# Performance work log

Measured on AMD Instinct MI355X. Metric: run time of the kernel, lower is better.

The kernel has to match this reference:

```python
import jax, jax.numpy as jnp
import numpy as np

N_NODES = 100000
N_EDGES = 3200000
N_GRAPHS = 64


def _seg_mean(vals, idx, num_segments):
    s = jax.ops.segment_sum(vals, idx, num_segments=num_segments)
    cnt = jax.ops.segment_sum(jnp.ones((vals.shape[0],), vals.dtype), idx,
                              num_segments=num_segments)
    return s / jnp.maximum(cnt, 1.0)[:, None]


def _gcn_layer(x, edge_index, edge_attr, Wc, bc, Wn):
    # center = lin1(x)
    center = x @ Wc + bc
    row, col = edge_index[0], edge_index[1]  # row = source (j), col = target (i)
    # degree computed over row indices (as in PyG degree(row))
    deg = jax.ops.segment_sum(jnp.ones((row.shape[0],), x.dtype), row,
                              num_segments=x.shape[0])
    deg_inv_sqrt = jnp.where(deg > 0, jax.lax.rsqrt(jnp.maximum(deg, 1.0)), 0.0)
    norm = deg_inv_sqrt[row] * deg_inv_sqrt[col]  # [E]
    # message: lin2(concat(x_j, edge_attr)) * norm
    msg = jnp.concatenate([x[row], edge_attr], axis=1) @ Wn  # [E, out]
    msg = msg * norm[:, None]
    # aggr='mean' at target nodes
    aggr = _seg_mean(msg, col, x.shape[0])
    return center + aggr


def setup_inputs() -> dict:
    key = jax.random.key(0)
    ks = jax.random.split(key, 12)
    x = jax.random.normal(ks[0], (N_NODES, 3), dtype=jnp.float32)
    edge_index = jax.random.randint(ks[1], (2, N_EDGES), 0, N_NODES, dtype=jnp.int64)
    edge_attr = jax.random.normal(ks[2], (N_EDGES, 2), dtype=jnp.float32)
    batch = jnp.sort(jax.random.randint(ks[3], (N_NODES,), 0, N_GRAPHS, dtype=jnp.int64))
    s = 0.2
    params = {
        'Wc1': jax.random.normal(ks[4], (3, 16), jnp.float32) * s,
        'bc1': jnp.zeros((16,), jnp.float32),
        'Wn1': jax.random.normal(ks[5], (5, 16), jnp.float32) * s,   # in+edge = 3+2
        'Wc2': jax.random.normal(ks[6], (16, 16), jnp.float32) * s,
        'bc2': jnp.zeros((16,), jnp.float32),
        'Wn2': jax.random.normal(ks[7], (18, 16), jnp.float32) * s,  # 16+2
        'Wl1': jax.random.normal(ks[8], (16, 16), jnp.float32) * s,
        'bl1': jnp.zeros((16,), jnp.float32),
        'Wl2': jax.random.normal(ks[9], (16, 2), jnp.float32) * s,
        'bl2': jnp.zeros((2,), jnp.float32),
    }
    return dict(x=x, edge_index=edge_index, edge_attr=edge_attr, batch=batch, **params)


def reference(x, edge_index, edge_attr, batch,
              Wc1, bc1, Wn1, Wc2, bc2, Wn2, Wl1, bl1, Wl2, bl2):
    h = _gcn_layer(x, edge_index, edge_attr, Wc1, bc1, Wn1)
    h = jax.nn.relu(h)  # dropout is identity in eval mode
    h = _gcn_layer(h, edge_index, edge_attr, Wc2, bc2, Wn2)
    h = jax.nn.relu(h)
    g = _seg_mean(h, batch, N_GRAPHS)          # global scatter_mean pooling [G,16]
    g = jax.nn.relu(g @ Wl1 + bl1)
    return g @ Wl2 + bl2                        # [G, 2]
```

## Files before the change

### kernel.cpp

```cpp
#include <hip/hip_runtime.h>

constexpr int TPBW = 1024;
constexpr int TPBS = 256;
constexpr int BSH  = 6;
constexpr int BKN  = 64;
constexpr int MAXB = 1600;
constexpr int CAP  = 2432;
constexpr int SBUF = 2432;
constexpr int ITER = 10;
constexpr int SIT  = 7;
constexpr int SEDG = SIT * TPBW;
constexpr int HWL  = 12800;

__device__ __forceinline__ unsigned short f2bf(float f) {
    unsigned u = __float_as_uint(f);
    u += 0x7FFFu + ((u >> 16) & 1u);
    return (unsigned short)(u >> 16);
}
__device__ __forceinline__ float bflo(unsigned u) {
    return __uint_as_float(u << 16);
}
__device__ __forceinline__ float bfhi(unsigned u) {
    return __uint_as_float(u & 0xFFFF0000u);
}

__global__ __launch_bounds__(TPBW)
void k_stage2(const int* __restrict__ ei, const float2* __restrict__ ea,
              int E, int NBKT, int W,
              int* __restrict__ gcnt, int2* __restrict__ staged,
              unsigned int* __restrict__ partialR) {
    __shared__ unsigned int lh[HWL];
    __shared__ int2 sb2[SEDG];
    __shared__ unsigned short sbk[SEDG];
    __shared__ int cl[MAXB], gb[MAXB], rs[MAXB + 1];
    __shared__ int tmp[1024];
    __shared__ int carry_s;
    const int p = blockIdx.x, t = threadIdx.x;
    for (int i = t; i < W; i += TPBW) lh[i] = 0;
    for (int b = t; b < NBKT; b += TPBW) cl[b] = 0;
    if (t == 0) carry_s = 0;
    __syncthreads();
    const int* colA = ei + E;
    const int s = p * SEDG, send = min(s + SEDG, E);
    int rid[SIT], eap[SIT], bk[SIT], rk[SIT];
#pragma unroll
    for (int k = 0; k < SIT; k++) {
        int e = s + t + k * TPBW;
        bk[k] = -1;
        if (e < send) {
            int r = ei[e], c = colA[e];
            atomicAdd(&lh[r >> 3], 1u << ((r & 7) * 4));
            int b = c >> BSH;
            float2 ev = ea[e];
            rid[k] = (r << BSH) | (c & (BKN - 1));
            eap[k] = (int)((unsigned)f2bf(ev.x) | ((unsigned)f2bf(ev.y) << 16));
            bk[k] = b;
            rk[k] = atomicAdd(&cl[b], 1);
        }
    }
    __syncthreads();
    for (int chunk = 0; chunk < NBKT; chunk += 1024) {
        int idx = chunk + t;
        int v = (idx < NBKT) ? cl[idx] : 0;
        tmp[t] = v;
        __syncthreads();
        for (int off = 1; off < 1024; off <<= 1) {
            int add = (t >= off) ? tmp[t - off] : 0;
            __syncthreads();
            tmp[t] += add;
            __syncthreads();
        }
        int incl = tmp[t];
        int carry = carry_s;
        if (idx < NBKT) rs[idx] = carry + incl - v;
        __syncthreads();
        if (t == 1023) carry_s = carry + incl;
        __syncthreads();
    }
    if (t == 0) rs[NBKT] = carry_s;
    __syncthreads();
    for (int b = t; b < NBKT; b += TPBW) {
        int c = cl[b];
        gb[b] = c ? atomicAdd(&gcnt[b], c) : 0;
    }
    __syncthreads();
#pragma unroll
    for (int k = 0; k < SIT; k++)
        if (bk[k] >= 0) {
            int slot = rs[bk[k]] + rk[k];
            sb2[slot] = make_int2(rid[k], eap[k]);
            sbk[slot] = (unsigned short)bk[k];
        }
    __syncthreads();
    const int total = rs[NBKT];
    for (int i = t; i < total; i += TPBW) {
        int b = sbk[i];
        int pos = gb[b] + (i - rs[b]);
        if (pos < CAP) staged[(size_t)b * CAP + pos] = sb2[i];
    }
    for (int w = t; w < W; w += TPBW) partialR[(size_t)p * W + w] = lh[w];
}

__global__ __launch_bounds__(512)
void k_xd(const unsigned int* __restrict__ partialR, int NP, int W, int N,
          const float* __restrict__ x,
          float* __restrict__ dis, float4* __restrict__ xd) {
    __shared__ unsigned int sA[8][64], sB[8][64];
    const int wloc = threadIdx.x & 63, lane = threadIdx.x >> 6;
    const int w = blockIdx.x * 64 + wloc;
    unsigned int accA = 0, accB = 0;
    if (w < W) {
        for (int p = lane; p < NP; p += 8) {
            unsigned int v = partialR[(size_t)p * W + w];
            accA += v & 0x0F0F0F0Fu;
            accB += (v >> 4) & 0x0F0F0F0Fu;
        }
    }
    sA[lane][wloc] = accA;
    sB[lane][wloc] = accB;
    __syncthreads();
    if (lane == 0 && w < W) {
#pragma unroll
        for (int l = 1; l < 8; l++) { accA += sA[l][wloc]; accB += sB[l][wloc]; }
        int d[8];
        d[0] = accA & 255; d[2] = (accA >> 8) & 255;
        d[4] = (accA >> 16) & 255; d[6] = accA >> 24;
        d[1] = accB & 255; d[3] = (accB >> 8) & 255;
        d[5] = (accB >> 16) & 255; d[7] = accB >> 24;
        const int n0 = w * 8;
#pragma unroll
        for (int k = 0; k < 8; k++) {
            int n = n0 + k;
            if (n < N) {
                float dv = d[k] ? rsqrtf((float)d[k]) : 0.f;
                dis[n] = dv;
                xd[n] = make_float4(x[3 * (size_t)n], x[3 * (size_t)n + 1],
                                    x[3 * (size_t)n + 2], dv);
            }
        }
    }
}

__global__ __launch_bounds__(TPBS)
void k_sortA(int2* __restrict__ staged, const int* __restrict__ gcnt,
             const float4* __restrict__ xd, int N,
             const float* __restrict__ Wc, const float* __restrict__ bc,
             const float* __restrict__ Wn,
             unsigned short* __restrict__ hb, unsigned short* __restrict__ hbs,
             float2* __restrict__ eaS,
             int* __restrict__ cnt, int* __restrict__ base, int* __restrict__ segN) {
    __shared__ int2 sbuf2[SBUF];
    __shared__ int lfill[BKN], lexc[BKN];
    __shared__ float sax[BKN], say[BKN], saz[BKN], se1[BKN], se2[BKN];
    __shared__ float sWc[48], sbc[16], sWn[80];
    __shared__ int stot;
    const int b = blockIdx.x, t = threadIdx.x;
    const size_t s0 = (size_t)b * CAP;
    const int c0 = b << BSH;
    int cb = gcnt[b]; if (cb > CAP) cb = CAP;
    if (t < BKN) lfill[t] = 0;
    if (t < 48) sWc[t] = Wc[t];
    if (t >= 64 && t < 80) sbc[t - 64] = bc[t - 64];
    if (t >= 128 && t < 208) sWn[t - 128] = Wn[t - 128];
    __syncthreads();
    int er[ITER], ep[ITER], rk[ITER];
#pragma unroll
    for (int k = 0; k < ITER; k++) {
        int e = t + k * TPBS;
        rk[k] = -1;
        if (e < cb) {
            int2 v = staged[s0 + e];
            int j = v.x & (BKN - 1);
            er[k] = (int)(((unsigned)v.x) >> BSH);
            ep[k] = v.y;
            rk[k] = atomicAdd(&lfill[j], 1) | (j << 16);
        }
    }
    __syncthreads();
    if (t < 64) {
        int v = lfill[t];
        int incl = v;
#pragma unroll
        for (int off = 1; off < 64; off <<= 1) {
            int up = __shfl_up(incl, off, 64);
            if (t >= off) incl += up;
        }
        lexc[t] = incl - v;
        if (t == 63) stot = incl;
    }
    __syncthreads();
#pragma unroll
    for (int k = 0; k < ITER; k++) {
        if (rk[k] >= 0) {
            int j = rk[k] >> 16, rr = rk[k] & 0xFFFF;
            sbuf2[lexc[j] + rr] = make_int2(er[k], ep[k]);
        }
    }
    __syncthreads();
    int tot = stot; if (tot > SBUF) tot = SBUF;
    const int grp = t >> 2, sub = t & 3;
    const int node = c0 + grp;
    float a0 = 0.f, a1 = 0.f, a2 = 0.f, b1 = 0.f, b2 = 0.f;
    {
        int e0 = lexc[grp], dg = lfill[grp];
        if (node < N) {
            for (int e = sub; e < dg; e += 8) {
                int2 ve0 = sbuf2[e0 + e];
                bool v1 = (e + 4) < dg;
                int2 ve1 = v1 ? sbuf2[e0 + e + 4] : ve0;
                float4 q0 = xd[ve0.x];
                float4 q1 = xd[ve1.x];
                float w0 = q0.w;
                float w1 = v1 ? q1.w : 0.f;
                a0 += w0 * q0.x + w1 * q1.x;
                a1 += w0 * q0.y + w1 * q1.y;
                a2 += w0 * q0.z + w1 * q1.z;
                b1 += w0 * bflo((unsigned)ve0.y) + w1 * bflo((unsigned)ve1.y);
                b2 += w0 * bfhi((unsigned)ve0.y) + w1 * bfhi((unsigned)ve1.y);
            }
        }
    }
    a0 += __shfl_down(a0, 2, 4); a0 += __shfl_down(a0, 1, 4);
    a1 += __shfl_down(a1, 2, 4); a1 += __shfl_down(a1, 1, 4);
    a2 += __shfl_down(a2, 2, 4); a2 += __shfl_down(a2, 1, 4);
    b1 += __shfl_down(b1, 2, 4); b1 += __shfl_down(b1, 1, 4);
    b2 += __shfl_down(b2, 2, 4); b2 += __shfl_down(b2, 1, 4);
    if (sub == 0) {
        sax[grp] = a0; say[grp] = a1; saz[grp] = a2;
        se1[grp] = b1; se2[grp] = b2;
    }
    {
        int* ridS = (int*)staged;
        for (int i = t; i < tot; i += TPBS) ridS[s0 * 2 + i] = sbuf2[i].x;
    }
    if (t == 0) segN[b] = tot;
    if (t < BKN) {
        int nd = c0 + t;
        if (nd < N) { cnt[nd] = lfill[t]; base[nd] = lexc[t]; }
    }
    __syncthreads();
    if (t < BKN) {
        int nd = c0 + t;
        if (nd < N) {
            float inv = 1.0f / fmaxf((float)lfill[t], 1.0f);
            float4 xq = xd[nd];
            float ldt = xq.w;
            float sc = ldt * inv;
            float m[5] = {sax[t] * sc, say[t] * sc, saz[t] * sc,
                          se1[t] * sc, se2[t] * sc};
            float xv[3] = {xq.x, xq.y, xq.z};
            float o[16];
#pragma unroll
            for (int k = 0; k < 16; k++) {
                float v = sbc[k];
#pragma unroll
                for (int j = 0; j < 3; j++) v += xv[j] * sWc[j * 16 + k];
#pragma unroll
                for (int j = 0; j < 5; j++) v += m[j] * sWn[j * 16 + k];
                o[k] = fmaxf(v, 0.0f);
            }
            unsigned ov[8], sv[8];
#pragma unroll
            for (int q = 0; q < 8; q++) {
                ov[q] = (unsigned)f2bf(o[2 * q]) | ((unsigned)f2bf(o[2 * q + 1]) << 16);
                sv[q] = (unsigned)f2bf(ldt * o[2 * q]) |
                        ((unsigned)f2bf(ldt * o[2 * q + 1]) << 16);
            }
            uint4* hp = (uint4*)(hb + 16 * (size_t)nd);
            hp[0] = make_uint4(ov[0], ov[1], ov[2], ov[3]);
            hp[1] = make_uint4(ov[4], ov[5], ov[6], ov[7]);
            uint4* hps = (uint4*)(hbs + 16 * (size_t)nd);
            hps[0] = make_uint4(sv[0], sv[1], sv[2], sv[3]);
            hps[1] = make_uint4(sv[4], sv[5], sv[6], sv[7]);
            eaS[nd] = make_float2(se1[t] * ldt, se2[t] * ldt);
        }
    }
}

__global__ __launch_bounds__(TPBS)
void k_g2(const int* __restrict__ ridS, const int* __restrict__ cnt,
          const int* __restrict__ base, const int* __restrict__ segN,
          const float* __restrict__ dis, const unsigned short* __restrict__ hb,
          const unsigned short* __restrict__ hbs,
          const float2* __restrict__ eaS, const int* __restrict__ batch, int N,
          const float* __restrict__ Wc, const float* __restrict__ bc,
          const float* __restrict__ Wn,
          float* __restrict__ pool, int* __restrict__ poolcnt) {
    __shared__ int sbuf[SBUF];
    __shared__ int lfill[BKN], lexc[BKN];
    __shared__ float smr[BKN][17];
    __shared__ float sWc[256], sbc[16], sWn[288], sp[1024];
    __shared__ int sc[64];
    const int b = blockIdx.x, t = threadIdx.x;
    const size_t s0 = (size_t)b * CAP * 2;
    const int c0 = b << BSH;
    if (t < BKN) {
        int nd = c0 + t;
        lfill[t] = (nd < N) ? cnt[nd] : 0;
        lexc[t]  = (nd < N) ? base[nd] : 0;
    }
    for (int k = t; k < 256; k += TPBS) sWc[k] = Wc[k];
    for (int k = t; k < 16;  k += TPBS) sbc[k] = bc[k];
    for (int k = t; k < 288; k += TPBS) sWn[k] = Wn[k];
    for (int k = t; k < 1024; k += TPBS) sp[k] = 0.f;
    if (t < 64) sc[t] = 0;
    int tot = segN[b];
    if (tot > SBUF) tot = SBUF;
    for (int i = t; i < tot; i += TPBS) sbuf[i] = ridS[s0 + i];
    __syncthreads();
    const int grp = t >> 2, sub = t & 3;
    const int node = c0 + grp;
    float mm[16];
#pragma unroll
    for (int k = 0; k < 16; k++) mm[k] = 0.f;
    if (node < N) {
        int e0 = lexc[grp], dg = lfill[grp];
        for (int e = sub; e < dg; e += 8) {
            int r0 = sbuf[e0 + e];
            bool v1 = (e + 4) < dg;
            int r1 = v1 ? sbuf[e0 + e + 4] : r0;
            const uint4* h0 = (const uint4*)(hbs + 16 * (size_t)r0);
            const uint4* h1 = (const uint4*)(hbs + 16 * (size_t)r1);
            uint4 A0 = h0[0], B0 = h0[1];
            uint4 A1 = h1[0], B1 = h1[1];
            float s1 = v1 ? 1.f : 0.f;
            mm[0]  += bflo(A0.x) + s1 * bflo(A1.x);
            mm[1]  += bfhi(A0.x) + s1 * bfhi(A1.x);
            mm[2]  += bflo(A0.y) + s1 * bflo(A1.y);
            mm[3]  += bfhi(A0.y) + s1 * bfhi(A1.y);
            mm[4]  += bflo(A0.z) + s1 * bflo(A1.z);
            mm[5]  += bfhi(A0.z) + s1 * bfhi(A1.z);
            mm[6]  += bflo(A0.w) + s1 * bflo(A1.w);
            mm[7]  += bfhi(A0.w) + s1 * bfhi(A1.w);
            mm[8]  += bflo(B0.x) + s1 * bflo(B1.x);
            mm[9]  += bfhi(B0.x) + s1 * bfhi(B1.x);
            mm[10] += bflo(B0.y) + s1 * bflo(B1.y);
            mm[11] += bfhi(B0.y) + s1 * bfhi(B1.y);
            mm[12] += bflo(B0.z) + s1 * bflo(B1.z);
            mm[13] += bfhi(B0.z) + s1 * bfhi(B1.z);
            mm[14] += bflo(B0.w) + s1 * bflo(B1.w);
            mm[15] += bfhi(B0.w) + s1 * bfhi(B1.w);
        }
    }
#pragma unroll
    for (int k = 0; k < 16; k++) {
        mm[k] += __shfl_down(mm[k], 2, 4);
        mm[k] += __shfl_down(mm[k], 1, 4);
    }
    if (sub == 0) {
#pragma unroll
        for (int k = 0; k < 16; k++) smr[grp][k] = mm[k];
    }
    __syncthreads();
    if (t < BKN) {
        int nd = c0 + t;
        if (nd < N) {
            float inv = 1.0f / fmaxf((float)lfill[t], 1.0f);
            float ldt = dis[nd];
            float scm = ldt * inv;
            float m[18];
#pragma unroll
            for (int k = 0; k < 16; k++) m[k] = smr[t][k] * scm;
            float2 es = eaS[nd];
            m[16] = es.x * inv; m[17] = es.y * inv;
            const uint4* hp = (const uint4*)(hb + 16 * (size_t)nd);
            uint4 A = hp[0], B = hp[1];
            float hv[16] = {bflo(A.x), bfhi(A.x), bflo(A.y), bfhi(A.y),
                            bflo(A.z), bfhi(A.z), bflo(A.w), bfhi(A.w),
                            bflo(B.x), bfhi(B.x), bflo(B.y), bfhi(B.y),
                            bflo(B.z), bfhi(B.z), bflo(B.w), bfhi(B.w)};
            int g = batch[nd];
            atomicAdd(&sc[g], 1);
#pragma unroll
            for (int k = 0; k < 16; k++) {
                float v = sbc[k];
#pragma unroll
                for (int j = 0; j < 16; j++) v += hv[j] * sWc[j * 16 + k];
#pragma unroll
                for (int j = 0; j < 18; j++) v += m[j] * sWn[j * 16 + k];
                v = fmaxf(v, 0.0f);
                unsafeAtomicAdd(&sp[g * 16 + k], v);
            }
        }
    }
    __syncthreads();
    for (int k = t; k < 1024; k += TPBS)
        if (sp[k] != 0.0f) unsafeAtomicAdd(&pool[k], sp[k]);
    if (t < 64 && sc[t]) atomicAdd(&poolcnt[t], sc[t]);
}

__global__ void k_final(const float* __restrict__ pool, const int* __restrict__ poolcnt,
                        const float* __restrict__ Wl1, const float* __restrict__ bl1,
                        const float* __restrict__ Wl2, const float* __restrict__ bl2,
                        float* __restrict__ out) {
    int g = threadIdx.x;
    if (g >= 64) return;
    float inv = 1.0f / fmaxf((float)poolcnt[g], 1.0f);
    float gv[16];
#pragma unroll
    for (int k = 0; k < 16; k++) gv[k] = pool[g * 16 + k] * inv;
    float t[16];
#pragma unroll
    for (int k = 0; k < 16; k++) {
        float v = bl1[k];
#pragma unroll
        for (int j = 0; j < 16; j++) v += gv[j] * Wl1[j * 16 + k];
        t[k] = fmaxf(v, 0.0f);
    }
    float o0 = bl2[0], o1 = bl2[1];
#pragma unroll
    for (int j = 0; j < 16; j++) {
        o0 += t[j] * Wl2[j * 2 + 0];
        o1 += t[j] * Wl2[j * 2 + 1];
    }
    out[2 * g + 0] = o0;
    out[2 * g + 1] = o1;
}

extern "C" void kernel_launch(void* const* d_in, const int* in_sizes, int n_in,
                              void* d_out, int out_size, void* d_ws, size_t ws_size,
                              hipStream_t stream) {
    const float* x     = (const float*)d_in[0];
    const int*   ei    = (const int*)  d_in[1];
    const float* ea    = (const float*)d_in[2];
    const int*   batch = (const int*)  d_in[3];
    const float* Wc1   = (const float*)d_in[4];
    const float* bc1   = (const float*)d_in[5];
    const float* Wn1   = (const float*)d_in[6];
    const float* Wc2   = (const float*)d_in[7];
    const float* bc2   = (const float*)d_in[8];
    const float* Wn2   = (const float*)d_in[9];
    const float* Wl1   = (const float*)d_in[10];
    const float* bl1   = (const float*)d_in[11];
    const float* Wl2   = (const float*)d_in[12];
    const float* bl2   = (const float*)d_in[13];
    float* out = (float*)d_out;

    const int N  = in_sizes[0] / 3;
    const int E  = in_sizes[1] / 2;
    const int NBKT = (N + BKN - 1) >> BSH;
    const int SGRID = (E + SEDG - 1) / SEDG;
    const int W = (N + 7) >> 3;

    char* ws = (char*)d_ws;
    size_t o = 0;
    auto alloc = [&](size_t bytes) {
        void* p = ws + o;
        o += (bytes + 255) & ~(size_t)255;
        return p;
    };
    float* pool    = (float*)alloc(64 * 16 * 4);
    int*   poolcnt = (int*)  alloc(64 * 4);
    int*   gcnt    = (int*)  alloc((size_t)NBKT * 4);
    size_t zbytes = o;
    float*  dis     = (float*)alloc((size_t)N * 4);
    float4* xd      = (float4*)alloc((size_t)N * 16);
    float2* eaS     = (float2*)alloc((size_t)N * 8);
    int*    cnt     = (int*)  alloc((size_t)N * 4);
    int*    base    = (int*)  alloc((size_t)N * 4);
    int*    segN    = (int*)  alloc((size_t)NBKT * 4);
    unsigned int* partialR = (unsigned int*)alloc((size_t)SGRID * W * 4);
    int2*   staged  = (int2*)alloc((size_t)NBKT * CAP * 8);
    unsigned short* hb  = (unsigned short*)alloc((size_t)N * 16 * 2);
    unsigned short* hbs = (unsigned short*)alloc((size_t)N * 16 * 2);
    (void)ws_size;

    hipMemsetAsync(d_ws, 0, zbytes, stream);

    k_stage2<<<SGRID, TPBW, 0, stream>>>(ei, (const float2*)ea, E, NBKT, W,
                                         gcnt, staged, partialR);
    k_xd    <<<(W + 63) / 64, 512, 0, stream>>>(partialR, SGRID, W, N, x, dis, xd);
    k_sortA <<<NBKT, TPBS, 0, stream>>>(staged, gcnt, xd, N,
                                        Wc1, bc1, Wn1, hb, hbs, eaS,
                                        cnt, base, segN);
    k_g2    <<<NBKT, TPBS, 0, stream>>>((const int*)staged, cnt, base, segN,
                                        dis, hb, hbs, eaS, batch, N,
                                        Wc2, bc2, Wn2, pool, poolcnt);
    k_final <<<1, 64, 0, stream>>>(pool, poolcnt, Wl1, bl1, Wl2, bl2, out);
}
```

Measured before the change: 229.4 us.

## Use wave-shuffle bucket scan and fold final MLP into last g2 block

Replaces the shared-memory Hillis-Steele prefix scan over bucket counts, which needed many block barriers, with a two-level wavefront shuffle scan where each thread handles two buckets. It also removes the separate k_final launch: the last k_g2 block to finish, found through an atomic done counter and threadfences, computes the pooled-mean MLP. This removes one kernel launch and its gap. The shuffle scan covers at most 2048 buckets, which is enough for NBKT of 1563.

```diff
diff --git a/kernel.cpp b/kernel.cpp
--- a/kernel.cpp
+++ b/kernel.cpp
@@ -32,13 +32,12 @@
     __shared__ unsigned int lh[HWL];
     __shared__ int2 sb2[SEDG];
     __shared__ unsigned short sbk[SEDG];
-    __shared__ int cl[MAXB], gb[MAXB], rs[MAXB + 1];
-    __shared__ int tmp[1024];
-    __shared__ int carry_s;
+    __shared__ int cl[MAXB], gb[MAXB], rs[MAXB];
+    __shared__ int wtot[16];
+    __shared__ int tot_s;
     const int p = blockIdx.x, t = threadIdx.x;
     for (int i = t; i < W; i += TPBW) lh[i] = 0;
     for (int b = t; b < NBKT; b += TPBW) cl[b] = 0;
-    if (t == 0) carry_s = 0;
     __syncthreads();
     const int* colA = ei + E;
     const int s = p * SEDG, send = min(s + SEDG, E);
@@ -59,25 +58,36 @@
         }
     }
     __syncthreads();
-    for (int chunk = 0; chunk < NBKT; chunk += 1024) {
-        int idx = chunk + t;
-        int v = (idx < NBKT) ? cl[idx] : 0;
-        tmp[t] = v;
+    {
+        const int i0 = 2 * t, i1 = 2 * t + 1;
+        const int a  = (i0 < NBKT) ? cl[i0] : 0;
+        const int bb = (i1 < NBKT) ? cl[i1] : 0;
+        const int sv = a + bb;
+        int incl = sv;
+        const int lane = t & 63, wid = t >> 6;
+#pragma unroll
+        for (int off = 1; off < 64; off <<= 1) {
+            int up = __shfl_up(incl, off, 64);
+            if (lane >= off) incl += up;
+        }
+        if (lane == 63) wtot[wid] = incl;
         __syncthreads();
-        for (int off = 1; off < 1024; off <<= 1) {
-            int add = (t >= off) ? tmp[t - off] : 0;
-            __syncthreads();
-            tmp[t] += add;
-            __syncthreads();
-        }
-        int incl = tmp[t];
-        int carry = carry_s;
-        if (idx < NBKT) rs[idx] = carry + incl - v;
+        if (t < 16) {
+            int v = wtot[t];
+            int inc2 = v;
+#pragma unroll
+            for (int off = 1; off < 16; off <<= 1) {
+                int up = __shfl_up(inc2, off, 16);
+                if (t >= off) inc2 += up;
+            }
+            wtot[t] = inc2 - v;
+            if (t == 15) tot_s = inc2;
+        }
         __syncthreads();
-        if (t == 1023) carry_s = carry + incl;
-        __syncthreads();
-    }
-    if (t == 0) rs[NBKT] = carry_s;
+        int exc = wtot[wid] + incl - sv;
+        if (i0 < NBKT) rs[i0] = exc;
+        if (i1 < NBKT) rs[i1] = exc + a;
+    }
     __syncthreads();
     for (int b = t; b < NBKT; b += TPBW) {
         int c = cl[b];
@@ -92,7 +102,7 @@
             sbk[slot] = (unsigned short)bk[k];
         }
     __syncthreads();
-    const int total = rs[NBKT];
+    const int total = tot_s;
     for (int i = t; i < total; i += TPBW) {
         int b = sbk[i];
         int pos = gb[b] + (i - rs[b]);
@@ -285,12 +295,17 @@
           const float2* __restrict__ eaS, const int* __restrict__ batch, int N,
           const float* __restrict__ Wc, const float* __restrict__ bc,
           const float* __restrict__ Wn,
-          float* __restrict__ pool, int* __restrict__ poolcnt) {
+          float* __restrict__ pool, int* __restrict__ poolcnt,
+          int* __restrict__ done,
+          const float* __restrict__ Wl1, const float* __restrict__ bl1,
+          const float* __restrict__ Wl2, const float* __restrict__ bl2,
+          float* __restrict__ out) {
     __shared__ int sbuf[SBUF];
     __shared__ int lfill[BKN], lexc[BKN];
     __shared__ float smr[BKN][17];
     __shared__ float sWc[256], sbc[16], sWn[288], sp[1024];
     __shared__ int sc[64];
+    __shared__ int lastF;
     const int b = blockIdx.x, t = threadIdx.x;
     const size_t s0 = (size_t)b * CAP * 2;
     const int c0 = b << BSH;
@@ -387,34 +402,41 @@
     for (int k = t; k < 1024; k += TPBS)
         if (sp[k] != 0.0f) unsafeAtomicAdd(&pool[k], sp[k]);
     if (t < 64 && sc[t]) atomicAdd(&poolcnt[t], sc[t]);
-}
-
-__global__ void k_final(const float* __restrict__ pool, const int* __restrict__ poolcnt,
-                        const float* __restrict__ Wl1, const float* __restrict__ bl1,
-                        const float* __restrict__ Wl2, const float* __restrict__ bl2,
-                        float* __restrict__ out) {
-    int g = threadIdx.x;
-    if (g >= 64) return;
-    float inv = 1.0f / fmaxf((float)poolcnt[g], 1.0f);
-    float gv[16];
-#pragma unroll
-    for (int k = 0; k < 16; k++) gv[k] = pool[g * 16 + k] * inv;
-    float t[16];
-#pragma unroll
-    for (int k = 0; k < 16; k++) {
-        float v = bl1[k];
-#pragma unroll
-        for (int j = 0; j < 16; j++) v += gv[j] * Wl1[j * 16 + k];
-        t[k] = fmaxf(v, 0.0f);
-    }
-    float o0 = bl2[0], o1 = bl2[1];
-#pragma unroll
-    for (int j = 0; j < 16; j++) {
-        o0 += t[j] * Wl2[j * 2 + 0];
-        o1 += t[j] * Wl2[j * 2 + 1];
-    }
-    out[2 * g + 0] = o0;
-    out[2 * g + 1] = o1;
+    __syncthreads();
+    if (t == 0) {
+        __threadfence();
+        int prev = atomicAdd(done, 1);
+        lastF = (prev == (int)gridDim.x - 1) ? 1 : 0;
+    }
+    __syncthreads();
+    if (lastF) {
+        __threadfence();
+        if (t < 64) {
+            volatile const float* vp  = pool;
+            volatile const int*   vpc = poolcnt;
+            int g = t;
+            float inv = 1.0f / fmaxf((float)vpc[g], 1.0f);
+            float gv[16];
+#pragma unroll
+            for (int k = 0; k < 16; k++) gv[k] = vp[g * 16 + k] * inv;
+            float tt[16];
+#pragma unroll
+            for (int k = 0; k < 16; k++) {
+                float v = bl1[k];
+#pragma unroll
+                for (int j = 0; j < 16; j++) v += gv[j] * Wl1[j * 16 + k];
+                tt[k] = fmaxf(v, 0.0f);
+            }
+            float o0 = bl2[0], o1 = bl2[1];
+#pragma unroll
+            for (int j = 0; j < 16; j++) {
+                o0 += tt[j] * Wl2[j * 2 + 0];
+                o1 += tt[j] * Wl2[j * 2 + 1];
+            }
+            out[2 * g + 0] = o0;
+            out[2 * g + 1] = o1;
+        }
+    }
 }
 
 extern "C" void kernel_launch(void* const* d_in, const int* in_sizes, int n_in,
@@ -452,6 +474,7 @@
     float* pool    = (float*)alloc(64 * 16 * 4);
     int*   poolcnt = (int*)  alloc(64 * 4);
     int*   gcnt    = (int*)  alloc((size_t)NBKT * 4);
+    int*   done    = (int*)  alloc(4);
     size_t zbytes = o;
     float*  dis     = (float*)alloc((size_t)N * 4);
     float4* xd      = (float4*)alloc((size_t)N * 16);
@@ -475,6 +498,6 @@
                                         cnt, base, segN);
     k_g2    <<<NBKT, TPBS, 0, stream>>>((const int*)staged, cnt, base, segN,
                                         dis, hb, hbs, eaS, batch, N,
-                                        Wc2, bc2, Wn2, pool, poolcnt);
-    k_final <<<1, 64, 0, stream>>>(pool, poolcnt, Wl1, bl1, Wl2, bl2, out);
-}
+                                        Wc2, bc2, Wn2, pool, poolcnt, done,
+                                        Wl1, bl1, Wl2, bl2, out);
+}
```

Result: slower. 250.3 us (+9.1%).
